# Kernel optimization log

Hardware: AMD Instinct MI355X
Metric: run time of the kernel (lower is better)

## Reference

```python
import jax, jax.numpy as jnp
import numpy as np

INTER = 32  # inter_channels = in_channels // 2


def conv1x1(x, w, b):
    # x: (b, c_in, h, w), w: (c_out, c_in), b: (c_out,)
    return jnp.einsum('bchw,oc->bohw', x, w) + b[None, :, None, None]


def setup_inputs() -> dict:
    key = jax.random.key(0)
    ks = jax.random.split(key, 12)
    B, C, H, W = 8, 64, 64, 64
    inter = INTER
    s_in = 1.0 / np.sqrt(C)      # torch conv default init scale
    s_int = 1.0 / np.sqrt(inter)
    return {
        'x': jax.random.normal(ks[0], (B, C, H, W), jnp.float32),
        'g_w': jax.random.normal(ks[1], (inter, C), jnp.float32) * s_in,
        'g_b': jax.random.normal(ks[2], (inter,), jnp.float32) * s_in,
        'theta_w': jax.random.normal(ks[3], (inter, C), jnp.float32) * s_in,
        'theta_b': jax.random.normal(ks[4], (inter,), jnp.float32) * s_in,
        'phi_w': jax.random.normal(ks[5], (inter, C), jnp.float32) * s_in,
        'phi_b': jax.random.normal(ks[6], (inter,), jnp.float32) * s_in,
        'W_w': jax.random.normal(ks[7], (C, inter), jnp.float32) * s_int,
        'W_b': jax.random.normal(ks[8], (C,), jnp.float32) * s_int,
        'Wz1_w': jax.random.normal(ks[9], (C, inter), jnp.float32) * s_int,
        'Wz1_b': jax.random.normal(ks[10], (C,), jnp.float32) * s_int,
        'mb': jax.random.normal(ks[11], (inter, 256), jnp.float32),
    }


def reference(x, g_w, g_b, theta_w, theta_b, phi_w, phi_b, W_w, W_b, Wz1_w, Wz1_b, mb):
    b, c, h, w = x.shape
    inter = g_w.shape[0]
    # 1x1 conv projections, flattened over spatial: N = h*w
    g_x = conv1x1(x, g_w, g_b).reshape(b, inter, -1)          # (b, ic, N)
    theta_x = conv1x1(x, theta_w, theta_b).reshape(b, inter, -1)
    phi_x = conv1x1(x, phi_w, phi_b).reshape(b, inter, -1)    # (b, ic, N)
    # non-local self-attention: f = theta^T @ phi, unscaled softmax
    f = jnp.einsum('bcn,bcm->bnm', theta_x, phi_x)            # (b, N, N)
    f_div_C = jax.nn.softmax(f, axis=-1)
    y = jnp.einsum('bnm,bcm->bcn', f_div_C, g_x)              # (b, ic, N)
    y = y.reshape(b, inter, h, w)
    W_y = conv1x1(y, W_w, W_b)                                # (b, c, h, w)
    # memory-bank cross-attention: phi^T @ mb, scaled softmax
    f1 = jnp.einsum('bcn,ck->bnk', phi_x, mb)                 # (b, N, 256)
    scale = jnp.float32(int(inter) ** (-0.5))
    f_div_C1 = jax.nn.softmax(f1 * scale, axis=-1)
    y1 = jnp.einsum('bnk,ck->bcn', f_div_C1, mb)              # (b, ic, N)
    y1 = y1.reshape(b, inter, h, w)
    W_y1 = conv1x1(y1, Wz1_w, Wz1_b)
    return W_y + x + W_y1
```

## Files before the change

kernel.cpp:

```cpp
#include <hip/hip_runtime.h>
#include <hip/hip_bf16.h>

#define N_POS 4096
#define C_IN 64
#define IC 32
#define L2E 1.4426950408889634f

typedef float f32x16 __attribute__((ext_vector_type(16)));
typedef short bf16x8 __attribute__((ext_vector_type(8)));
typedef unsigned int uint;
typedef uint uint4v __attribute__((ext_vector_type(4)));
typedef unsigned short ushort;

static __device__ __forceinline__ ushort f2bf(float f) {
    __hip_bfloat16 h = __float2bfloat16(f);
    return __builtin_bit_cast(ushort, h);
}
static __device__ __forceinline__ float bf2f(ushort u) {
    uint v = ((uint)u) << 16;
    return __builtin_bit_cast(float, v);
}
static __device__ __forceinline__ uint packbf2(float lo, float hi) {
    return (uint)f2bf(lo) | ((uint)f2bf(hi) << 16);
}
static __device__ __forceinline__ uint packtrunc(float lo, float hi) {
    uint l = __builtin_bit_cast(uint, lo);
    uint h = __builtin_bit_cast(uint, hi);
    return (l >> 16) | (h & 0xffff0000u);
}

__global__ __launch_bounds__(128) void proj_kernel(
    const float* __restrict__ x,
    const float* __restrict__ g_w, const float* __restrict__ g_b,
    const float* __restrict__ th_w, const float* __restrict__ th_b,
    const float* __restrict__ ph_w, const float* __restrict__ ph_b,
    ushort* __restrict__ gcn, ushort* __restrict__ tht, ushort* __restrict__ pht)
{
    int gy = blockIdx.y;
    int pj = gy >> 1, half = gy & 1;
    const float* wsrc = (pj == 0) ? g_w : (pj == 1) ? th_w : ph_w;
    const float* bsrc = (pj == 0) ? g_b : (pj == 1) ? th_b : ph_b;
    __shared__ float w[16][64];
    __shared__ float bias[16];
    int tid = threadIdx.x;
    for (int i = tid; i < 1024; i += 128) w[i >> 6][i & 63] = wsrc[half * 1024 + i];
    if (tid < 16) bias[tid] = bsrc[half * 16 + tid];
    __syncthreads();

    int ng = blockIdx.x * 128 + tid;
    int b = ng >> 12, n = ng & 4095;
    const float* xb = x + (size_t)b * C_IN * N_POS + n;
    float xr[64];
    #pragma unroll
    for (int c = 0; c < 64; c++) xr[c] = xb[(size_t)c * N_POS];

    float acc[16];
    #pragma unroll
    for (int o = 0; o < 16; o++) {
        float a = bias[o];
        const float4* w4 = (const float4*)w[o];
        #pragma unroll
        for (int c4 = 0; c4 < 16; c4++) {
            float4 wv = w4[c4];
            a += wv.x * xr[c4*4+0] + wv.y * xr[c4*4+1]
               + wv.z * xr[c4*4+2] + wv.w * xr[c4*4+3];
        }
        if (pj == 1) a *= L2E;
        acc[o] = a;
    }

    if (pj == 0) {
        #pragma unroll
        for (int c = 0; c < 16; c++)
            gcn[((size_t)(b * IC + half * 16 + c)) * N_POS + n] = f2bf(acc[c]);
    } else {
        ushort* dst = ((pj == 1) ? tht : pht) + ((size_t)(b * N_POS + n)) * IC + half * 16;
        uint4v pk0, pk1;
        #pragma unroll
        for (int i = 0; i < 4; i++) pk0[i] = packbf2(acc[2*i], acc[2*i+1]);
        #pragma unroll
        for (int i = 0; i < 4; i++) pk1[i] = packbf2(acc[8+2*i], acc[8+2*i+1]);
        *(uint4v*)dst = pk0;
        *(uint4v*)(dst + 8) = pk1;
    }
}

__global__ __launch_bounds__(256) void mbprep_kernel(
    const float* __restrict__ mb, ushort* __restrict__ mbt,
    ushort* __restrict__ mbb)
{
    int i = blockIdx.x * 256 + threadIdx.x;
    int c = i >> 8, k = i & 255;
    float v = mb[i];
    mbb[i] = f2bf(v);
    mbt[k * 32 + c] = f2bf(v * (0.17677669529663687f * L2E));
}

__global__ __launch_bounds__(256) void attn_kernel(
    const ushort* __restrict__ tht, const ushort* __restrict__ pht,
    const ushort* __restrict__ gcn, float* __restrict__ yp,
    float* __restrict__ dnm)
{
    __shared__ float redY[4][2][32][32];
    __shared__ float redD[4][2][32];
    int tid = threadIdx.x;
    int s = tid >> 6, lane = tid & 63;
    int bid = blockIdx.x;
    int b = bid & 7;
    int rest = bid >> 3;
    int qp = rest >> 1;
    int half = rest & 1;
    int q0 = qp * 64;
    int mbase = (half * 4 + s) * 512;
    int cl = lane & 31, h = lane >> 5;
    int t4 = (cl >> 2) & 3;
    int pcl = (t4 == 1 || t4 == 2) ? (cl ^ 12) : cl;

    const ushort* thpA = tht + ((size_t)(b * N_POS + q0 + cl)) * IC + 8 * h;
    bf16x8 thA0 = *(const bf16x8*)thpA;
    bf16x8 thA1 = *(const bf16x8*)(thpA + 16);
    const ushort* thpB = thpA + 32 * IC;
    bf16x8 thB0 = *(const bf16x8*)thpB;
    bf16x8 thB1 = *(const bf16x8*)(thpB + 16);

    const ushort* phbase = pht + (size_t)b * N_POS * IC;
    const ushort* gbase  = gcn + ((size_t)(b * IC + cl)) * N_POS;

    f32x16 yA0, yA1, yB0, yB1, zero;
    #pragma unroll
    for (int i = 0; i < 16; i++) {
        yA0[i] = 0.f; yA1[i] = 0.f; yB0[i] = 0.f; yB1[i] = 0.f; zero[i] = 0.f;
    }
    float sumeA = 0.f, sumeB = 0.f;

    #pragma unroll 2
    for (int mt = 0; mt < 16; ++mt) {
        int m0 = mbase + mt * 32;
        const ushort* php = phbase + ((size_t)(m0 + pcl)) * IC + 8 * h;
        bf16x8 ph0 = *(const bf16x8*)php;
        bf16x8 ph1 = *(const bf16x8*)(php + 16);
        const ushort* gp = gbase + m0 + 8 * h;
        bf16x8 g0 = *(const bf16x8*)gp;
        bf16x8 g1 = *(const bf16x8*)(gp + 16);

        f32x16 sv = __builtin_amdgcn_mfma_f32_32x32x16_bf16(ph0, thA0, zero, 0, 0, 0);
        sv = __builtin_amdgcn_mfma_f32_32x32x16_bf16(ph1, thA1, sv, 0, 0, 0);
        uint wA[8];
        #pragma unroll
        for (int i = 0; i < 8; i++) {
            float p0 = __builtin_amdgcn_exp2f(sv[2*i]);
            float p1 = __builtin_amdgcn_exp2f(sv[2*i+1]);
            sumeA += p0 + p1;
            wA[i] = packtrunc(p0, p1);
        }
        f32x16 sw = __builtin_amdgcn_mfma_f32_32x32x16_bf16(ph0, thB0, zero, 0, 0, 0);
        sw = __builtin_amdgcn_mfma_f32_32x32x16_bf16(ph1, thB1, sw, 0, 0, 0);
        uint wB[8];
        #pragma unroll
        for (int i = 0; i < 8; i++) {
            float p0 = __builtin_amdgcn_exp2f(sw[2*i]);
            float p1 = __builtin_amdgcn_exp2f(sw[2*i+1]);
            sumeB += p0 + p1;
            wB[i] = packtrunc(p0, p1);
        }

        uint4v aA0, aA1, aB0, aB1;
        aA0[0] = wA[0]; aA0[1] = wA[1]; aA0[2] = wA[2]; aA0[3] = wA[3];
        aA1[0] = wA[4]; aA1[1] = wA[5]; aA1[2] = wA[6]; aA1[3] = wA[7];
        aB0[0] = wB[0]; aB0[1] = wB[1]; aB0[2] = wB[2]; aB0[3] = wB[3];
        aB1[0] = wB[4]; aB1[1] = wB[5]; aB1[2] = wB[6]; aB1[3] = wB[7];

        yA0 = __builtin_amdgcn_mfma_f32_32x32x16_bf16(
            __builtin_bit_cast(bf16x8, aA0), g0, yA0, 0, 0, 0);
        yA1 = __builtin_amdgcn_mfma_f32_32x32x16_bf16(
            __builtin_bit_cast(bf16x8, aA1), g1, yA1, 0, 0, 0);
        yB0 = __builtin_amdgcn_mfma_f32_32x32x16_bf16(
            __builtin_bit_cast(bf16x8, aB0), g0, yB0, 0, 0, 0);
        yB1 = __builtin_amdgcn_mfma_f32_32x32x16_bf16(
            __builtin_bit_cast(bf16x8, aB1), g1, yB1, 0, 0, 0);
    }

    sumeA += __shfl_xor(sumeA, 32);
    sumeB += __shfl_xor(sumeB, 32);
    if (lane < 32) { redD[s][0][cl] = sumeA; redD[s][1][cl] = sumeB; }
    #pragma unroll
    for (int r = 0; r < 16; r++) {
        int q = (r & 3) + 8 * (r >> 2) + 4 * h;
        redY[s][0][q][cl] = yA0[r] + yA1[r];
        redY[s][1][q][cl] = yB0[r] + yB1[r];
    }
    __syncthreads();

    int q = tid >> 3, c4 = tid & 7;
    #pragma unroll
    for (int j = 0; j < 2; j++) {
        float den = redD[0][j][q] + redD[1][j][q] + redD[2][j][q] + redD[3][j][q];
        float4 v0 = *(const float4*)&redY[0][j][q][c4 * 4];
        float4 v1 = *(const float4*)&redY[1][j][q][c4 * 4];
        float4 v2 = *(const float4*)&redY[2][j][q][c4 * 4];
        float4 v3 = *(const float4*)&redY[3][j][q][c4 * 4];
        float4 vv;
        vv.x = v0.x + v1.x + v2.x + v3.x;
        vv.y = v0.y + v1.y + v2.y + v3.y;
        vv.z = v0.z + v1.z + v2.z + v3.z;
        vv.w = v0.w + v1.w + v2.w + v3.w;
        size_t t = ((size_t)(b * 128 + qp * 2 + j)) * 2 + half;
        *(float4*)(yp + t * 1024 + q * 32 + c4 * 4) = vv;
        if (c4 == 0) dnm[t * 32 + q] = den;
    }
}

__global__ __launch_bounds__(256) void mbout_kernel(
    const ushort* __restrict__ pht, const ushort* __restrict__ mbt,
    const ushort* __restrict__ mbb, const float* __restrict__ yp,
    const float* __restrict__ dnm, const float* __restrict__ x,
    const float* __restrict__ Ww, const float* __restrict__ Wb,
    const float* __restrict__ Wzw, const float* __restrict__ Wzb,
    float* __restrict__ out)
{
    __shared__ float sW[64][32], sWz[64][32];
    __shared__ float sb[64];
    __shared__ float ly1[128][33];
    int tid = threadIdx.x;
    int bid = blockIdx.x;
    int b = bid & 7, grp = bid >> 3;
    int n0 = grp * 128;

    for (int i = tid; i < 2048; i += 256) {
        int o = i >> 5, c = i & 31;
        sW[o][c]  = Ww[i];
        sWz[o][c] = Wzw[i];
    }
    if (tid < 64) sb[tid] = Wb[tid] + Wzb[tid];

    int s = tid >> 6, lane = tid & 63;
    int cl = lane & 31, h = lane >> 5;
    int t4 = (cl >> 2) & 3;
    int pcl = (t4 == 1 || t4 == 2) ? (cl ^ 12) : cl;
    int q0 = n0 + s * 32;

    const ushort* php = pht + ((size_t)(b * N_POS + q0 + cl)) * IC + 8 * h;
    bf16x8 qf0 = *(const bf16x8*)php;
    bf16x8 qf1 = *(const bf16x8*)(php + 16);

    f32x16 yaccA, yaccB, zero;
    #pragma unroll
    for (int i = 0; i < 16; i++) { yaccA[i] = 0.f; yaccB[i] = 0.f; zero[i] = 0.f; }
    float sume = 0.f;

    #pragma unroll 2
    for (int kt = 0; kt < 8; ++kt) {
        int k0 = kt * 32;
        const ushort* ap = mbt + ((size_t)(k0 + pcl)) * IC + 8 * h;
        bf16x8 af0 = *(const bf16x8*)ap;
        bf16x8 af1 = *(const bf16x8*)(ap + 16);
        const ushort* bp = mbb + (size_t)cl * 256 + k0 + 8 * h;
        bf16x8 bf0 = *(const bf16x8*)bp;
        bf16x8 bf1 = *(const bf16x8*)(bp + 16);

        f32x16 sv = __builtin_amdgcn_mfma_f32_32x32x16_bf16(af0, qf0, zero, 0, 0, 0);
        sv = __builtin_amdgcn_mfma_f32_32x32x16_bf16(af1, qf1, sv, 0, 0, 0);

        uint w[8];
        #pragma unroll
        for (int i = 0; i < 8; i++) {
            float p0 = __builtin_amdgcn_exp2f(sv[2*i]);
            float p1 = __builtin_amdgcn_exp2f(sv[2*i+1]);
            sume += p0 + p1;
            w[i] = packtrunc(p0, p1);
        }
        uint4v a0, a1;
        a0[0] = w[0]; a0[1] = w[1]; a0[2] = w[2]; a0[3] = w[3];
        a1[0] = w[4]; a1[1] = w[5]; a1[2] = w[6]; a1[3] = w[7];

        yaccA = __builtin_amdgcn_mfma_f32_32x32x16_bf16(
            __builtin_bit_cast(bf16x8, a0), bf0, yaccA, 0, 0, 0);
        yaccB = __builtin_amdgcn_mfma_f32_32x32x16_bf16(
            __builtin_bit_cast(bf16x8, a1), bf1, yaccB, 0, 0, 0);
    }

    sume += __shfl_xor(sume, 32);
    #pragma unroll
    for (int r = 0; r < 16; r++) {
        int q = (r & 3) + 8 * (r >> 2) + 4 * h;
        float d = __shfl(sume, q);
        ly1[s * 32 + q][cl] = (yaccA[r] + yaccB[r]) / d;
    }
    __syncthreads();

    int nl = tid >> 1, oh = tid & 1;
    int n = n0 + nl;
    int qt = n >> 5, q = n & 31;
    size_t t0 = ((size_t)(b * 128 + qt)) * 2;
    float inv = 1.f / (dnm[t0 * 32 + q] + dnm[t0 * 32 + 32 + q]);

    const float* yp0 = yp + t0 * 1024 + q * 32;
    const float* yp1 = yp0 + 1024;
    float yv[32], y1v[32];
    #pragma unroll
    for (int c4 = 0; c4 < 8; c4++) {
        float4 v0 = ((const float4*)yp0)[c4];
        float4 v1 = ((const float4*)yp1)[c4];
        yv[c4*4+0] = (v0.x + v1.x) * inv;
        yv[c4*4+1] = (v0.y + v1.y) * inv;
        yv[c4*4+2] = (v0.z + v1.z) * inv;
        yv[c4*4+3] = (v0.w + v1.w) * inv;
    }
    #pragma unroll
    for (int c = 0; c < 32; c++) y1v[c] = ly1[nl][c];

    const float* xb = x   + ((size_t)(b * C_IN + oh * 32)) * N_POS + n;
    float*       ob = out + ((size_t)(b * C_IN + oh * 32)) * N_POS + n;
    for (int o = 0; o < 32; o++) {
        float acc = sb[oh * 32 + o] + xb[(size_t)o * N_POS];
        const float4* w4  = (const float4*)sW[oh * 32 + o];
        const float4* wz4 = (const float4*)sWz[oh * 32 + o];
        #pragma unroll
        for (int c4 = 0; c4 < 8; c4++) {
            float4 a = w4[c4], z = wz4[c4];
            acc += a.x * yv[c4*4+0] + a.y * yv[c4*4+1] + a.z * yv[c4*4+2] + a.w * yv[c4*4+3];
            acc += z.x * y1v[c4*4+0] + z.y * y1v[c4*4+1] + z.z * y1v[c4*4+2] + z.w * y1v[c4*4+3];
        }
        ob[(size_t)o * N_POS] = acc;
    }
}

extern "C" void kernel_launch(void* const* d_in, const int* in_sizes, int n_in,
                              void* d_out, int out_size, void* d_ws, size_t ws_size,
                              hipStream_t stream) {
    const float* x    = (const float*)d_in[0];
    const float* g_w  = (const float*)d_in[1];
    const float* g_b  = (const float*)d_in[2];
    const float* th_w = (const float*)d_in[3];
    const float* th_b = (const float*)d_in[4];
    const float* ph_w = (const float*)d_in[5];
    const float* ph_b = (const float*)d_in[6];
    const float* W_w  = (const float*)d_in[7];
    const float* W_b  = (const float*)d_in[8];
    const float* Wz_w = (const float*)d_in[9];
    const float* Wz_b = (const float*)d_in[10];
    const float* mb   = (const float*)d_in[11];
    float* out = (float*)d_out;

    char* w = (char*)d_ws;
    ushort* tht = (ushort*)w;
    ushort* pht = (ushort*)(w + (2u << 20));
    ushort* gcn = (ushort*)(w + (4u << 20));
    ushort* mbt = (ushort*)(w + (6u << 20));
    ushort* mbb = (ushort*)(w + (6u << 20) + 16384);
    float*  yp  = (float*)(w + (9u << 20));
    float*  dnm = (float*)(w + (17u << 20));

    proj_kernel<<<dim3(256, 6), 128, 0, stream>>>(x, g_w, g_b, th_w, th_b,
                                                  ph_w, ph_b, gcn, tht, pht);
    mbprep_kernel<<<32, 256, 0, stream>>>(mb, mbt, mbb);
    attn_kernel<<<1024, 256, 0, stream>>>(tht, pht, gcn, yp, dnm);
    mbout_kernel<<<256, 256, 0, stream>>>(pht, mbt, mbb, yp, dnm, x,
                                          W_w, W_b, Wz_w, Wz_b, out);
}
```

Baseline: 88.74 us.

## Fold mb prep into projection kernel and split mbout over memory-bank halves

The memory-bank preprocessing moves into the projection kernel, which removes one kernel launch. The mbout kernel now covers 64 positions per block over 512 blocks, and the four waves split the 256 memory-bank keys in two halves, with partial sums combined through shared memory. The output projection work is divided so each thread handles 16 output channels. packtrunc uses a single byte-permute instruction. More blocks and split-K should give better occupancy on the final kernel, at the cost of reloading weights per block and extra shared-memory reduction.

```diff
diff --git a/kernel.cpp b/kernel.cpp
--- a/kernel.cpp
+++ b/kernel.cpp
@@ -24,9 +24,8 @@
     return (uint)f2bf(lo) | ((uint)f2bf(hi) << 16);
 }
 static __device__ __forceinline__ uint packtrunc(float lo, float hi) {
-    uint l = __builtin_bit_cast(uint, lo);
-    uint h = __builtin_bit_cast(uint, hi);
-    return (l >> 16) | (h & 0xffff0000u);
+    return __builtin_amdgcn_perm(__builtin_bit_cast(uint, hi),
+                                 __builtin_bit_cast(uint, lo), 0x07060302u);
 }
 
 __global__ __launch_bounds__(128) void proj_kernel(
@@ -34,7 +33,9 @@
     const float* __restrict__ g_w, const float* __restrict__ g_b,
     const float* __restrict__ th_w, const float* __restrict__ th_b,
     const float* __restrict__ ph_w, const float* __restrict__ ph_b,
-    ushort* __restrict__ gcn, ushort* __restrict__ tht, ushort* __restrict__ pht)
+    const float* __restrict__ mb,
+    ushort* __restrict__ gcn, ushort* __restrict__ tht, ushort* __restrict__ pht,
+    ushort* __restrict__ mbt, ushort* __restrict__ mbb)
 {
     int gy = blockIdx.y;
     int pj = gy >> 1, half = gy & 1;
@@ -83,17 +84,14 @@
         *(uint4v*)dst = pk0;
         *(uint4v*)(dst + 8) = pk1;
     }
-}
-
-__global__ __launch_bounds__(256) void mbprep_kernel(
-    const float* __restrict__ mb, ushort* __restrict__ mbt,
-    ushort* __restrict__ mbb)
-{
-    int i = blockIdx.x * 256 + threadIdx.x;
-    int c = i >> 8, k = i & 255;
-    float v = mb[i];
-    mbb[i] = f2bf(v);
-    mbt[k * 32 + c] = f2bf(v * (0.17677669529663687f * L2E));
+
+    if (gy == 0 && blockIdx.x < 64) {
+        int i = blockIdx.x * 128 + tid;
+        int c = i >> 8, k = i & 255;
+        float v = mb[i];
+        mbb[i] = f2bf(v);
+        mbt[k * 32 + c] = f2bf(v * (0.17677669529663687f * L2E));
+    }
 }
 
 __global__ __launch_bounds__(256) void attn_kernel(
@@ -220,24 +218,25 @@
 {
     __shared__ float sW[64][32], sWz[64][32];
     __shared__ float sb[64];
-    __shared__ float ly1[128][33];
+    __shared__ float ly1p[4][32][36];
+    __shared__ float sumeL[4][32];
     int tid = threadIdx.x;
     int bid = blockIdx.x;
     int b = bid & 7, grp = bid >> 3;
-    int n0 = grp * 128;
+    int n0 = grp * 64;
 
     for (int i = tid; i < 2048; i += 256) {
-        int o = i >> 5, c = i & 31;
-        sW[o][c]  = Ww[i];
-        sWz[o][c] = Wzw[i];
+        sW[i >> 5][i & 31]  = Ww[i];
+        sWz[i >> 5][i & 31] = Wzw[i];
     }
     if (tid < 64) sb[tid] = Wb[tid] + Wzb[tid];
 
     int s = tid >> 6, lane = tid & 63;
+    int j = s & 1, kh = s >> 1;
+    int q0 = n0 + j * 32;
     int cl = lane & 31, h = lane >> 5;
     int t4 = (cl >> 2) & 3;
     int pcl = (t4 == 1 || t4 == 2) ? (cl ^ 12) : cl;
-    int q0 = n0 + s * 32;
 
     const ushort* php = pht + ((size_t)(b * N_POS + q0 + cl)) * IC + 8 * h;
     bf16x8 qf0 = *(const bf16x8*)php;
@@ -248,9 +247,9 @@
     for (int i = 0; i < 16; i++) { yaccA[i] = 0.f; yaccB[i] = 0.f; zero[i] = 0.f; }
     float sume = 0.f;
 
-    #pragma unroll 2
-    for (int kt = 0; kt < 8; ++kt) {
-        int k0 = kt * 32;
+    #pragma unroll
+    for (int kt = 0; kt < 4; ++kt) {
+        int k0 = (kh * 4 + kt) * 32;
         const ushort* ap = mbt + ((size_t)(k0 + pcl)) * IC + 8 * h;
         bf16x8 af0 = *(const bf16x8*)ap;
         bf16x8 af1 = *(const bf16x8*)(ap + 16);
@@ -280,23 +279,36 @@
     }
 
     sume += __shfl_xor(sume, 32);
+    if (lane < 32) sumeL[s][cl] = sume;
     #pragma unroll
     for (int r = 0; r < 16; r++) {
         int q = (r & 3) + 8 * (r >> 2) + 4 * h;
-        float d = __shfl(sume, q);
-        ly1[s * 32 + q][cl] = (yaccA[r] + yaccB[r]) / d;
+        ly1p[s][q][cl] = yaccA[r] + yaccB[r];
     }
     __syncthreads();
 
-    int nl = tid >> 1, oh = tid & 1;
-    int n = n0 + nl;
-    int qt = n >> 5, q = n & 31;
+    int obase = (s & 1) * 32 + (s >> 1) * 16;
+    int n = n0 + lane;
+    int jj = lane >> 5, q = lane & 31;
+
+    float inv1 = 1.f / (sumeL[jj][q] + sumeL[2 + jj][q]);
+    float y1v[32];
+    #pragma unroll
+    for (int c4 = 0; c4 < 8; c4++) {
+        float4 p0 = *(const float4*)&ly1p[jj][q][c4 * 4];
+        float4 p1 = *(const float4*)&ly1p[2 + jj][q][c4 * 4];
+        y1v[c4*4+0] = (p0.x + p1.x) * inv1;
+        y1v[c4*4+1] = (p0.y + p1.y) * inv1;
+        y1v[c4*4+2] = (p0.z + p1.z) * inv1;
+        y1v[c4*4+3] = (p0.w + p1.w) * inv1;
+    }
+
+    int qt = n >> 5;
     size_t t0 = ((size_t)(b * 128 + qt)) * 2;
     float inv = 1.f / (dnm[t0 * 32 + q] + dnm[t0 * 32 + 32 + q]);
-
     const float* yp0 = yp + t0 * 1024 + q * 32;
     const float* yp1 = yp0 + 1024;
-    float yv[32], y1v[32];
+    float yv[32];
     #pragma unroll
     for (int c4 = 0; c4 < 8; c4++) {
         float4 v0 = ((const float4*)yp0)[c4];
@@ -306,15 +318,13 @@
         yv[c4*4+2] = (v0.z + v1.z) * inv;
         yv[c4*4+3] = (v0.w + v1.w) * inv;
     }
-    #pragma unroll
-    for (int c = 0; c < 32; c++) y1v[c] = ly1[nl][c];
-
-    const float* xb = x   + ((size_t)(b * C_IN + oh * 32)) * N_POS + n;
-    float*       ob = out + ((size_t)(b * C_IN + oh * 32)) * N_POS + n;
-    for (int o = 0; o < 32; o++) {
-        float acc = sb[oh * 32 + o] + xb[(size_t)o * N_POS];
-        const float4* w4  = (const float4*)sW[oh * 32 + o];
-        const float4* wz4 = (const float4*)sWz[oh * 32 + o];
+
+    const float* xb = x   + ((size_t)(b * C_IN + obase)) * N_POS + n;
+    float*       ob = out + ((size_t)(b * C_IN + obase)) * N_POS + n;
+    for (int o = 0; o < 16; o++) {
+        float acc = sb[obase + o] + xb[(size_t)o * N_POS];
+        const float4* w4  = (const float4*)sW[obase + o];
+        const float4* wz4 = (const float4*)sWz[obase + o];
         #pragma unroll
         for (int c4 = 0; c4 < 8; c4++) {
             float4 a = w4[c4], z = wz4[c4];
@@ -352,9 +362,9 @@
     float*  dnm = (float*)(w + (17u << 20));
 
     proj_kernel<<<dim3(256, 6), 128, 0, stream>>>(x, g_w, g_b, th_w, th_b,
-                                                  ph_w, ph_b, gcn, tht, pht);
-    mbprep_kernel<<<32, 256, 0, stream>>>(mb, mbt, mbb);
+                                                  ph_w, ph_b, mb,
+                                                  gcn, tht, pht, mbt, mbb);
     attn_kernel<<<1024, 256, 0, stream>>>(tht, pht, gcn, yp, dnm);
-    mbout_kernel<<<256, 256, 0, stream>>>(pht, mbt, mbb, yp, dnm, x,
+    mbout_kernel<<<512, 256, 0, stream>>>(pht, mbt, mbb, yp, dnm, x,
                                           W_w, W_b, Wz_w, Wz_b, out);
 }
```

Result: faster. 78.07 us (-12.0%).
